# Performance work log

Measured on AMD Instinct MI355X. Metric: run time of the kernel, lower is better.

The kernel has to match this reference:

```python
import jax, jax.numpy as jnp
import numpy as np
from jax import lax

S, D_IN, D_FC, H_LSTM, H_RNN, D_OUT = 16384, 6, 20, 48, 24, 2


def _lstm_layer(seq, Wih, Whh, bih, bhh):
    # seq: [S, d_in]; PyTorch gate order: i, f, g, o
    H = Whh.shape[1]
    xW = seq @ Wih.T + (bih + bhh)  # [S, 4H] precomputed input projections

    def step(carry, xw):
        h, c = carry
        g = xw + h @ Whh.T
        i = jax.nn.sigmoid(g[:H])
        f = jax.nn.sigmoid(g[H:2 * H])
        gg = jnp.tanh(g[2 * H:3 * H])
        o = jax.nn.sigmoid(g[3 * H:])
        c = f * c + i * gg
        h = o * jnp.tanh(c)
        return (h, c), h

    z = jnp.zeros((H,), seq.dtype)
    _, hs = lax.scan(step, (z, z), xW)
    return hs  # [S, H]


def _rnn_layer(seq, Wih, Whh, bih, bhh):
    H = Whh.shape[1]
    xW = seq @ Wih.T + (bih + bhh)

    def step(h, xw):
        h = jnp.tanh(xw + h @ Whh.T)
        return h, h

    _, hs = lax.scan(step, jnp.zeros((H,), seq.dtype), xW)
    return hs


def setup_inputs() -> dict:
    key = jax.random.key(0)
    ks = iter(jax.random.split(key, 32))

    def p(shape, fan_in):
        s = 1.0 / np.sqrt(fan_in)
        return jax.random.uniform(next(ks), shape, jnp.float32, -s, s)

    inp = {"x": jax.random.normal(next(ks), (S, D_IN), jnp.float32)}
    inp["fc1_W"] = p((D_FC, D_IN), D_IN)
    inp["fc1_b"] = p((D_FC,), D_IN)
    inp["fc2_W"] = p((D_FC, D_FC), D_FC)
    inp["fc2_b"] = p((D_FC,), D_FC)
    # LSTM layer 0: input 20 -> hidden 48
    inp["lstm0_Wih"] = p((4 * H_LSTM, D_FC), H_LSTM)
    inp["lstm0_Whh"] = p((4 * H_LSTM, H_LSTM), H_LSTM)
    inp["lstm0_bih"] = p((4 * H_LSTM,), H_LSTM)
    inp["lstm0_bhh"] = p((4 * H_LSTM,), H_LSTM)
    # LSTM layers 1..4: input 48 -> hidden 48, stacked
    inp["lstmr_Wih"] = p((4, 4 * H_LSTM, H_LSTM), H_LSTM)
    inp["lstmr_Whh"] = p((4, 4 * H_LSTM, H_LSTM), H_LSTM)
    inp["lstmr_bih"] = p((4, 4 * H_LSTM), H_LSTM)
    inp["lstmr_bhh"] = p((4, 4 * H_LSTM), H_LSTM)
    # RNN layer 0: 48 -> 24, layer 1: 24 -> 24
    inp["rnn0_Wih"] = p((H_RNN, H_LSTM), H_RNN)
    inp["rnn0_Whh"] = p((H_RNN, H_RNN), H_RNN)
    inp["rnn0_bih"] = p((H_RNN,), H_RNN)
    inp["rnn0_bhh"] = p((H_RNN,), H_RNN)
    inp["rnn1_Wih"] = p((H_RNN, H_RNN), H_RNN)
    inp["rnn1_Whh"] = p((H_RNN, H_RNN), H_RNN)
    inp["rnn1_bih"] = p((H_RNN,), H_RNN)
    inp["rnn1_bhh"] = p((H_RNN,), H_RNN)
    inp["fc4_W"] = p((D_OUT, H_RNN), H_RNN)
    inp["fc4_b"] = p((D_OUT,), H_RNN)
    return inp


def reference(x, fc1_W, fc1_b, fc2_W, fc2_b,
              lstm0_Wih, lstm0_Whh, lstm0_bih, lstm0_bhh,
              lstmr_Wih, lstmr_Whh, lstmr_bih, lstmr_bhh,
              rnn0_Wih, rnn0_Whh, rnn0_bih, rnn0_bhh,
              rnn1_Wih, rnn1_Whh, rnn1_bih, rnn1_bhh,
              fc4_W, fc4_b):
    h = jax.nn.relu(x @ fc1_W.T + fc1_b)
    h = jax.nn.relu(h @ fc2_W.T + fc2_b)
    h = _lstm_layer(h, lstm0_Wih, lstm0_Whh, lstm0_bih, lstm0_bhh)
    for l in range(4):  # fixed small layer loop
        h = _lstm_layer(h, lstmr_Wih[l], lstmr_Whh[l], lstmr_bih[l], lstmr_bhh[l])
    h = _rnn_layer(h, rnn0_Wih, rnn0_Whh, rnn0_bih, rnn0_bhh)
    h = _rnn_layer(h, rnn1_Wih, rnn1_Whh, rnn1_bih, rnn1_bhh)
    h = jax.nn.relu(h)
    out = h @ fc4_W.T + fc4_b  # [S, 2]
    return out[None]  # [1, S, 2] matching batch_first torch output
```

## Files before the change

### kernel.cpp

```cpp
#include <hip/hip_runtime.h>
#include <hip/hip_bf16.h>

#define S_LEN 16384
#define N_IN 23
#define CH2 32
#define NCH2 (S_LEN / CH2)
#define RING_D 8

typedef float v2f __attribute__((ext_vector_type(2)));
typedef _Float16 h2v __attribute__((ext_vector_type(2)));

__device__ __forceinline__ float fsig(float x) {
    return __builtin_amdgcn_rcpf(1.f + __expf(-x));
}
__device__ __forceinline__ float ftanh_fast(float x) {
    float e = __expf(-2.f * fabsf(x));
    float r = (1.f - e) * __builtin_amdgcn_rcpf(1.f + e);
    return x >= 0.f ? r : -r;
}
__device__ __forceinline__ float rlane(float v, int k) {
    return __uint_as_float(__builtin_amdgcn_readlane(__float_as_uint(v), k));
}
__device__ __forceinline__ h2v rlane_h2(h2v v, int k) {
    int b;
    __builtin_memcpy(&b, &v, 4);
    b = __builtin_amdgcn_readlane(b, k);
    h2v r;
    __builtin_memcpy(&r, &b, 4);
    return r;
}
__device__ __forceinline__ h2v pack_h2(float a, float b) {
    auto p = __builtin_amdgcn_cvt_pkrtz(a, b);
    h2v r;
    __builtin_memcpy(&r, &p, 4);
    return r;
}
__device__ __forceinline__ float dpp_xor1(float v) {
    int b = __float_as_int(v);
    int r = __builtin_amdgcn_update_dpp(b, b, 0xB1, 0xF, 0xF, false);
    return __int_as_float(r);
}

#if __has_builtin(__builtin_amdgcn_fdot2)
__device__ __forceinline__ float fdot2_hw(h2v w, h2v h, float acc) {
    return __builtin_amdgcn_fdot2(w, h, acc, false);
}
#define FDOT2(w, h, acc) fdot2_hw((w), (h), (acc))
#else
__device__ __forceinline__ float fdot2_sw(h2v w, h2v h, float acc) {
    return acc + (float)w.x * (float)h.x + (float)w.y * (float)h.y;
}
#define FDOT2(w, h, acc) fdot2_sw((w), (h), (acc))
#endif

__global__ void detect_kernel(const void* probe, int nsamp, int* flag)
{
    if (blockIdx.x == 0 && threadIdx.x == 0) {
        const unsigned short* p = (const unsigned short*)probe;
        int isbf16 = 1;
        for (int i = 0; i < nsamp; i++) {
            float v = __uint_as_float(((unsigned int)p[i]) << 16);
            if (!(fabsf(v) < 1e4f)) { isbf16 = 0; break; }
        }
        *flag = isbf16;
    }
}

struct IngestArgs {
    const void* src[N_IN];
    float*      dst[N_IN];
    int         n[N_IN];
};

__global__ void ingest_kernel(IngestArgs args, const int* __restrict__ flag)
{
    const int isbf16 = *flag;
    const int tid    = blockIdx.x * blockDim.x + threadIdx.x;
    const int stride = gridDim.x * blockDim.x;
    for (int i = 0; i < N_IN; i++) {
        const int n = args.n[i];
        float* dst  = args.dst[i];
        if (isbf16) {
            const unsigned short* s = (const unsigned short*)args.src[i];
            for (int j = tid; j < n; j += stride)
                dst[j] = __uint_as_float(((unsigned int)s[j]) << 16);
        } else {
            const float* s = (const float*)args.src[i];
            for (int j = tid; j < n; j += stride)
                dst[j] = s[j];
        }
    }
}

__global__ void init_kernel(int* prog)
{
    int t = threadIdx.x;
    if (t < 1024) prog[t] = 0;
}

__global__ void fc12_kernel(const float* __restrict__ x,
                            const float* __restrict__ W1, const float* __restrict__ b1,
                            const float* __restrict__ W2, const float* __restrict__ b2,
                            float* __restrict__ h2out)
{
    int s = blockIdx.x * blockDim.x + threadIdx.x;
    if (s >= S_LEN) return;
    float xin[6];
#pragma unroll
    for (int k = 0; k < 6; k++) xin[k] = x[s * 6 + k];
    float h1[20];
#pragma unroll
    for (int j = 0; j < 20; j++) {
        float a = b1[j];
#pragma unroll
        for (int k = 0; k < 6; k++) a += W1[j * 6 + k] * xin[k];
        h1[j] = a > 0.f ? a : 0.f;
    }
#pragma unroll
    for (int j = 0; j < 20; j++) {
        float a = b2[j];
#pragma unroll
        for (int k = 0; k < 20; k++) a += W2[j * 20 + k] * h1[k];
        h2out[s * 20 + j] = a > 0.f ? a : 0.f;
    }
}

template <int DIN, int NG, bool TRANS>
__device__ void producer_block(const float* __restrict__ in,
                               const float* __restrict__ Wih,
                               const float* __restrict__ bih,
                               const float* __restrict__ bhh,
                               float* __restrict__ ring,
                               int* my_prog, int* in_prog, int* cons_prog,
                               float* smem)
{
    constexpr int GR  = NG / 3;
    constexpr int GS  = 256 / GR;
    constexpr int SLT = CH2 / GS;

    const int t  = threadIdx.x;
    const int rg = t % GR;
    const int sg = t / GR;

    float* in_sh = smem;
    float* xw_sh = smem + CH2 * DIN;

    float w[3][DIN];
    float bs[3];
    int cellr[3], partr[3];
#pragma unroll
    for (int r = 0; r < 3; r++) {
        const int row = rg * 3 + r;
#pragma unroll
        for (int k = 0; k < DIN; k++) w[r][k] = Wih[row * DIN + k];
        bs[r] = bih[row] + bhh[row];
        cellr[r] = row % 48;
        partr[r] = row / 48;
    }

    const float4* x4 = (const float4*)in_sh;

    for (int c = 0; c < NCH2; c++) {
        if (t == 0) {
            if (in_prog) {
                while (__hip_atomic_load(in_prog, __ATOMIC_ACQUIRE, __HIP_MEMORY_SCOPE_AGENT) < c + 1)
                    __builtin_amdgcn_s_sleep(1);
            }
            if (c >= RING_D) {
                while (__hip_atomic_load(cons_prog, __ATOMIC_ACQUIRE, __HIP_MEMORY_SCOPE_AGENT) < c - RING_D + 1)
                    __builtin_amdgcn_s_sleep(1);
            }
        }
        __syncthreads();
        {
            const float4* gsrc = (const float4*)(in + (size_t)c * CH2 * DIN);
            float4* ldst = (float4*)in_sh;
            for (int i = t; i < CH2 * DIN / 4; i += 256) ldst[i] = gsrc[i];
        }
        __syncthreads();

#pragma unroll
        for (int i = 0; i < SLT; i++) {
            const int sl = sg * SLT + i;
            float a0 = bs[0], a1 = bs[1], a2 = bs[2];
#pragma unroll
            for (int k = 0; k < DIN / 4; k++) {
                float4 xv = x4[sl * (DIN / 4) + k];
                a0 += w[0][4 * k + 0] * xv.x; a0 += w[0][4 * k + 1] * xv.y;
                a0 += w[0][4 * k + 2] * xv.z; a0 += w[0][4 * k + 3] * xv.w;
                a1 += w[1][4 * k + 0] * xv.x; a1 += w[1][4 * k + 1] * xv.y;
                a1 += w[1][4 * k + 2] * xv.z; a1 += w[1][4 * k + 3] * xv.w;
                a2 += w[2][4 * k + 0] * xv.x; a2 += w[2][4 * k + 1] * xv.y;
                a2 += w[2][4 * k + 2] * xv.z; a2 += w[2][4 * k + 3] * xv.w;
            }
            if (TRANS) {
                xw_sh[(sl * 48 + cellr[0]) * 4 + partr[0]] = a0;
                xw_sh[(sl * 48 + cellr[1]) * 4 + partr[1]] = a1;
                xw_sh[(sl * 48 + cellr[2]) * 4 + partr[2]] = a2;
            } else {
                xw_sh[sl * NG + rg * 3 + 0] = a0;
                xw_sh[sl * NG + rg * 3 + 1] = a1;
                xw_sh[sl * NG + rg * 3 + 2] = a2;
            }
        }
        __syncthreads();
        {
            const float4* lsrc = (const float4*)xw_sh;
            float4* gdst = (float4*)(ring + (size_t)(c % RING_D) * CH2 * NG);
            for (int i = t; i < CH2 * NG / 4; i += 256) gdst[i] = lsrc[i];
        }
        __syncthreads();
        if (t == 0)
            __hip_atomic_store(my_prog, c + 1, __ATOMIC_RELEASE, __HIP_MEMORY_SCOPE_AGENT);
    }
}

__device__ void lstm_scan(const float* __restrict__ Whh,
                          const float* __restrict__ ring,
                          float* __restrict__ hseq,
                          int* my_prog, int* prod_prog, float* smem)
{
    const int t = threadIdx.x;
    const int j = (t < 48) ? t : 47;
    float* xw_buf = smem;
    float* hh_buf = smem + 12288;

    h2v wI[24], wF[24], wG[24], wO[24];
    if (t < 64) {
#pragma unroll
        for (int k = 0; k < 24; k++) {
            wI[k] = pack_h2(Whh[j * 48 + 2 * k],         Whh[j * 48 + 2 * k + 1]);
            wF[k] = pack_h2(Whh[(48 + j) * 48 + 2 * k],  Whh[(48 + j) * 48 + 2 * k + 1]);
            wG[k] = pack_h2(Whh[(96 + j) * 48 + 2 * k],  Whh[(96 + j) * 48 + 2 * k + 1]);
            wO[k] = pack_h2(Whh[(144 + j) * 48 + 2 * k], Whh[(144 + j) * 48 + 2 * k + 1]);
        }
    }
    float hvec = 0.f, ccell = 0.f;

    if (t >= 128) {
        while (__hip_atomic_load(prod_prog, __ATOMIC_ACQUIRE, __HIP_MEMORY_SCOPE_AGENT) < 1)
            __builtin_amdgcn_s_sleep(8);
        const float4* g = (const float4*)ring;
        float4* d = (float4*)xw_buf;
        for (int i = t - 128; i < CH2 * 48; i += 128) d[i] = g[i];
    }
    __syncthreads();

    for (int c = 0; c < NCH2; c++) {
        if (t < 64) {
            const float4* xf = (const float4*)(xw_buf + (c & 1) * (CH2 * 192));
            float* hh = hh_buf + (c & 1) * (CH2 * 48);
            float4 xw4 = xf[j];
            for (int sl = 0; sl < CH2; sl++) {
                float4 nxt = xf[(sl + 1 < CH2 ? sl + 1 : sl) * 48 + j];
                float hn = dpp_xor1(hvec);
                h2v hp = pack_h2(hvec, hn);
                float aI0 = xw4.x, aF0 = xw4.y, aG0 = xw4.z, aO0 = xw4.w;
                float aI1 = 0.f, aF1 = 0.f, aG1 = 0.f, aO1 = 0.f;
#pragma unroll
                for (int kp = 0; kp < 12; kp++) {
                    h2v hb = rlane_h2(hp, 2 * kp);
                    aI0 = FDOT2(wI[kp], hb, aI0);
                    aF0 = FDOT2(wF[kp], hb, aF0);
                    aG0 = FDOT2(wG[kp], hb, aG0);
                    aO0 = FDOT2(wO[kp], hb, aO0);
                }
#pragma unroll
                for (int kp = 12; kp < 24; kp++) {
                    h2v hb = rlane_h2(hp, 2 * kp);
                    aI1 = FDOT2(wI[kp], hb, aI1);
                    aF1 = FDOT2(wF[kp], hb, aF1);
                    aG1 = FDOT2(wG[kp], hb, aG1);
                    aO1 = FDOT2(wO[kp], hb, aO1);
                }
                float iv = fsig(aI0 + aI1);
                float fv = fsig(aF0 + aF1);
                float gv = 2.f * fsig(2.f * (aG0 + aG1)) - 1.f;
                ccell = fv * ccell + iv * gv;
                float eO = __expf(-(aO0 + aO1));
                float eC = __expf(-2.f * fabsf(ccell));
                float r  = (1.f - eC) * __builtin_amdgcn_rcpf((1.f + eO) * (1.f + eC));
                float h  = __int_as_float(__float_as_int(r) ^
                                          (__float_as_int(ccell) & 0x80000000));
                hvec = h;
                if (t < 48) hh[sl * 48 + t] = h;
                xw4 = nxt;
            }
        } else if (t < 128) {
            if (c >= 1) {
                const float4* s4 = (const float4*)(hh_buf + ((c - 1) & 1) * (CH2 * 48));
                float4* d4 = (float4*)(hseq + (size_t)(c - 1) * CH2 * 48);
                for (int i = t - 64; i < CH2 * 12; i += 64) d4[i] = s4[i];
                if (t == 64)
                    __hip_atomic_store(my_prog, c, __ATOMIC_RELEASE, __HIP_MEMORY_SCOPE_AGENT);
            }
        } else {
            if (c + 1 < NCH2) {
                while (__hip_atomic_load(prod_prog, __ATOMIC_ACQUIRE, __HIP_MEMORY_SCOPE_AGENT) < c + 2)
                    __builtin_amdgcn_s_sleep(8);
                const float4* g = (const float4*)(ring + (size_t)((c + 1) % RING_D) * CH2 * 192);
                float4* d = (float4*)(xw_buf + ((c + 1) & 1) * (CH2 * 192));
                for (int i = t - 128; i < CH2 * 48; i += 128) d[i] = g[i];
            }
        }
        __syncthreads();
    }
    if (t >= 64 && t < 128) {
        const float4* s4 = (const float4*)(hh_buf + ((NCH2 - 1) & 1) * (CH2 * 48));
        float4* d4 = (float4*)(hseq + (size_t)(NCH2 - 1) * CH2 * 48);
        for (int i = t - 64; i < CH2 * 12; i += 64) d4[i] = s4[i];
        if (t == 64)
            __hip_atomic_store(my_prog, NCH2, __ATOMIC_RELEASE, __HIP_MEMORY_SCOPE_AGENT);
    }
}

__device__ void rnn_scan(const float* __restrict__ Whh,
                         const float* __restrict__ ring,
                         float* __restrict__ hseq,
                         int* my_prog, int* prod_prog, float* smem)
{
    const int t = threadIdx.x;
    float* xw_buf = smem;
    float* hh_buf = smem + 1536;

    float whh[24];
    if (t < 24) {
#pragma unroll
        for (int k = 0; k < 24; k++) whh[k] = Whh[t * 24 + k];
    }
    float hvec = 0.f;

    if (t >= 128) {
        while (__hip_atomic_load(prod_prog, __ATOMIC_ACQUIRE, __HIP_MEMORY_SCOPE_AGENT) < 1)
            __builtin_amdgcn_s_sleep(8);
        const float4* g = (const float4*)ring;
        float4* d = (float4*)xw_buf;
        for (int i = t - 128; i < CH2 * 6; i += 128) d[i] = g[i];
    }
    __syncthreads();

    for (int c = 0; c < NCH2; c++) {
        if (t < 64) {
            const float* xwc = xw_buf + (c & 1) * (CH2 * 24);
            float* hh = hh_buf + (c & 1) * (CH2 * 24);
            float xwv = (t < 24) ? xwc[t] : 0.f;
            for (int sl = 0; sl < CH2; sl++) {
                float nxtx = (t < 24) ? xwc[((sl + 1 < CH2) ? sl + 1 : sl) * 24 + t] : 0.f;
                float a0 = xwv, a1 = 0.f, a2 = 0.f, a3 = 0.f;
#pragma unroll
                for (int k = 0; k < 24; k += 4) {
                    a0 += rlane(hvec, k + 0) * whh[k + 0];
                    a1 += rlane(hvec, k + 1) * whh[k + 1];
                    a2 += rlane(hvec, k + 2) * whh[k + 2];
                    a3 += rlane(hvec, k + 3) * whh[k + 3];
                }
                float h = ftanh_fast((a0 + a1) + (a2 + a3));
                if (t < 24) {
                    hvec = h;
                    hh[sl * 24 + t] = h;
                }
                xwv = nxtx;
            }
        } else if (t < 128) {
            if (c >= 1) {
                const float4* s4 = (const float4*)(hh_buf + ((c - 1) & 1) * (CH2 * 24));
                float4* d4 = (float4*)(hseq + (size_t)(c - 1) * CH2 * 24);
                for (int i = t - 64; i < CH2 * 6; i += 64) d4[i] = s4[i];
                if (t == 64)
                    __hip_atomic_store(my_prog, c, __ATOMIC_RELEASE, __HIP_MEMORY_SCOPE_AGENT);
            }
        } else {
            if (c + 1 < NCH2) {
                while (__hip_atomic_load(prod_prog, __ATOMIC_ACQUIRE, __HIP_MEMORY_SCOPE_AGENT) < c + 2)
                    __builtin_amdgcn_s_sleep(8);
                const float4* g = (const float4*)(ring + (size_t)((c + 1) % RING_D) * CH2 * 24);
                float4* d = (float4*)(xw_buf + ((c + 1) & 1) * (CH2 * 24));
                for (int i = t - 128; i < CH2 * 6; i += 128) d[i] = g[i];
            }
        }
        __syncthreads();
    }
    if (t >= 64 && t < 128) {
        const float4* s4 = (const float4*)(hh_buf + ((NCH2 - 1) & 1) * (CH2 * 24));
        float4* d4 = (float4*)(hseq + (size_t)(NCH2 - 1) * CH2 * 24);
        for (int i = t - 64; i < CH2 * 6; i += 64) d4[i] = s4[i];
        if (t == 64)
            __hip_atomic_store(my_prog, NCH2, __ATOMIC_RELEASE, __HIP_MEMORY_SCOPE_AGENT);
    }
}

struct PipeArgs {
    const float* h2;
    const float* l0_Wih; const float* l0_Whh; const float* l0_bih; const float* l0_bhh;
    const float* lr_Wih; const float* lr_Whh; const float* lr_bih; const float* lr_bhh;
    const float* r0_Wih; const float* r0_Whh; const float* r0_bih; const float* r0_bhh;
    const float* r1_Wih; const float* r1_Whh; const float* r1_bih; const float* r1_bhh;
    float* seq0; float* seq1; float* seq2; float* seq3; float* seq4;
    float* rnnA; float* rnnB;
    float* ring[7];
    int* prog;
};

__global__ void __launch_bounds__(256, 1) pipeline_kernel(PipeArgs a)
{
    __shared__ __align__(16) float smem[15360];
    const int b = blockIdx.x;
    const float* seqin[7] = {a.h2, a.seq0, a.seq1, a.seq2, a.seq3, a.seq4, a.rnnA};
    float* seqout[7] = {a.seq0, a.seq1, a.seq2, a.seq3, a.seq4, a.rnnA, a.rnnB};
    int* sp[7]; int* pp[7];
    for (int l = 0; l < 7; l++) { sp[l] = a.prog + l * 64; pp[l] = a.prog + (8 + l) * 64; }

    if (b < 7) {
        const int l = b;
        int* inp = (l == 0) ? nullptr : sp[l - 1];
        if (l == 0) {
            producer_block<20, 192, true>(a.h2, a.l0_Wih, a.l0_bih, a.l0_bhh,
                                          a.ring[0], pp[0], inp, sp[0], smem);
        } else if (l <= 4) {
            producer_block<48, 192, true>(seqin[l],
                                          a.lr_Wih + (size_t)(l - 1) * 192 * 48,
                                          a.lr_bih + (size_t)(l - 1) * 192,
                                          a.lr_bhh + (size_t)(l - 1) * 192,
                                          a.ring[l], pp[l], inp, sp[l], smem);
        } else if (l == 5) {
            producer_block<48, 24, false>(a.seq4, a.r0_Wih, a.r0_bih, a.r0_bhh,
                                          a.ring[5], pp[5], inp, sp[5], smem);
        } else {
            producer_block<24, 24, false>(a.rnnA, a.r1_Wih, a.r1_bih, a.r1_bhh,
                                          a.ring[6], pp[6], inp, sp[6], smem);
        }
    } else {
        const int l = b - 7;
        if (l == 0) {
            lstm_scan(a.l0_Whh, a.ring[0], seqout[0], sp[0], pp[0], smem);
        } else if (l <= 4) {
            lstm_scan(a.lr_Whh + (size_t)(l - 1) * 192 * 48,
                      a.ring[l], seqout[l], sp[l], pp[l], smem);
        } else if (l == 5) {
            rnn_scan(a.r0_Whh, a.ring[5], seqout[5], sp[5], pp[5], smem);
        } else {
            rnn_scan(a.r1_Whh, a.ring[6], seqout[6], sp[6], pp[6], smem);
        }
    }
}

__global__ void out_kernel(const float* __restrict__ hin,
                           const float* __restrict__ W,
                           const float* __restrict__ b,
                           void* __restrict__ out,
                           const int* __restrict__ flag)
{
    int s = blockIdx.x * blockDim.x + threadIdx.x;
    if (s >= S_LEN) return;
    const int isbf16 = *flag;
    float h[24];
#pragma unroll
    for (int k = 0; k < 24; k++) {
        float v = hin[s * 24 + k];
        h[k] = v > 0.f ? v : 0.f;
    }
#pragma unroll
    for (int j = 0; j < 2; j++) {
        float a = b[j];
#pragma unroll
        for (int k = 0; k < 24; k++) a += W[j * 24 + k] * h[k];
        if (isbf16) ((__hip_bfloat16*)out)[s * 2 + j] = __float2bfloat16(a);
        else        ((float*)out)[s * 2 + j] = a;
    }
}

extern "C" void kernel_launch(void* const* d_in, const int* in_sizes, int n_in,
                              void* d_out, int out_size, void* d_ws, size_t ws_size,
                              hipStream_t stream)
{
    int*   ip    = (int*)d_ws;
    int*   flag  = ip;
    int*   prog  = ip + 256;
    float* ws    = (float*)d_ws;
    float* conv0 = ws + 4096;

    IngestArgs ia;
    float* conv[N_IN];
    {
        float* p = conv0;
        for (int i = 0; i < N_IN; i++) {
            conv[i] = p;
            ia.src[i] = d_in[i];
            ia.dst[i] = p;
            ia.n[i]   = in_sizes[i];
            p += in_sizes[i];
        }
    }
    float* h2   = conv0 + 191000;
    float* seq0 = h2 + 327680;
    float* seq1 = seq0 + 786432;
    float* seq2 = seq1 + 786432;
    float* seq3 = seq2 + 786432;
    float* seq4 = seq3 + 786432;
    float* rnnA = seq4 + 786432;
    float* rnnB = rnnA + 393216;
    float* rbase = rnnB + 393216;
    float* ring[7];
    {
        float* p = rbase;
        for (int l = 0; l < 5; l++) { ring[l] = p; p += RING_D * CH2 * 192; }
        for (int l = 5; l < 7; l++) { ring[l] = p; p += RING_D * CH2 * 24;  }
    }

    const int TPB = 256;
    const int NB  = S_LEN / TPB;

    detect_kernel<<<1, 64, 0, stream>>>(d_in[1], in_sizes[1], flag);
    ingest_kernel<<<128, 256, 0, stream>>>(ia, flag);
    init_kernel<<<1, 1024, 0, stream>>>(prog);

    fc12_kernel<<<NB, TPB, 0, stream>>>(conv[0], conv[1], conv[2], conv[3], conv[4], h2);

    PipeArgs pa;
    pa.h2 = h2;
    pa.l0_Wih = conv[5];  pa.l0_Whh = conv[6];  pa.l0_bih = conv[7];  pa.l0_bhh = conv[8];
    pa.lr_Wih = conv[9];  pa.lr_Whh = conv[10]; pa.lr_bih = conv[11]; pa.lr_bhh = conv[12];
    pa.r0_Wih = conv[13]; pa.r0_Whh = conv[14]; pa.r0_bih = conv[15]; pa.r0_bhh = conv[16];
    pa.r1_Wih = conv[17]; pa.r1_Whh = conv[18]; pa.r1_bih = conv[19]; pa.r1_bhh = conv[20];
    pa.seq0 = seq0; pa.seq1 = seq1; pa.seq2 = seq2; pa.seq3 = seq3; pa.seq4 = seq4;
    pa.rnnA = rnnA; pa.rnnB = rnnB;
    for (int l = 0; l < 7; l++) pa.ring[l] = ring[l];
    pa.prog = prog;

    pipeline_kernel<<<14, 256, 0, stream>>>(pa);

    out_kernel<<<NB, TPB, 0, stream>>>(rnnB, conv[21], conv[22], d_out, flag);
}
```

Measured before the change: 5.604 ms.

## Fold log2e scaling into LSTM weights, use exp2, and pad xw LDS layout

Pre-multiplies the input and recurrent LSTM weights and biases by log2(e) (twice that for the g gate) so the serial recurrence can call hardware exp2 directly. It also merges the i and g gate reciprocals into one rcp. Separately, it pads the shared-memory xw buffer by one float4 every 16 entries to avoid LDS bank conflicts, which grows shared memory. The goal is fewer instructions on the latency-bound recurrent critical path, at the cost of extra fp16 rounding on the scaled weights.

```diff
diff --git a/kernel.cpp b/kernel.cpp
--- a/kernel.cpp
+++ b/kernel.cpp
@@ -7,9 +7,21 @@
 #define NCH2 (S_LEN / CH2)
 #define RING_D 8
 
+#define XW_PAR_F4 1632
+#define XW_FLOATS (2 * XW_PAR_F4 * 4)
+#define L2E   1.442695041f
+#define TWO_L2E 2.885390082f
+
 typedef float v2f __attribute__((ext_vector_type(2)));
 typedef _Float16 h2v __attribute__((ext_vector_type(2)));
 
+__device__ __forceinline__ float fexp2(float x) {
+#if __has_builtin(__builtin_amdgcn_exp2f)
+    return __builtin_amdgcn_exp2f(x);
+#else
+    return exp2f(x);
+#endif
+}
 __device__ __forceinline__ float fsig(float x) {
     return __builtin_amdgcn_rcpf(1.f + __expf(-x));
 }
@@ -151,9 +163,10 @@
 #pragma unroll
     for (int r = 0; r < 3; r++) {
         const int row = rg * 3 + r;
-#pragma unroll
-        for (int k = 0; k < DIN; k++) w[r][k] = Wih[row * DIN + k];
-        bs[r] = bih[row] + bhh[row];
+        const float fac = TRANS ? ((row / 48) == 2 ? TWO_L2E : L2E) : 1.f;
+#pragma unroll
+        for (int k = 0; k < DIN; k++) w[r][k] = Wih[row * DIN + k] * fac;
+        bs[r] = (bih[row] + bhh[row]) * fac;
         cellr[r] = row % 48;
         partr[r] = row / 48;
     }
@@ -223,18 +236,19 @@
     const int t = threadIdx.x;
     const int j = (t < 48) ? t : 47;
     float* xw_buf = smem;
-    float* hh_buf = smem + 12288;
+    float* hh_buf = smem + XW_FLOATS;
 
     h2v wI[24], wF[24], wG[24], wO[24];
     if (t < 64) {
 #pragma unroll
         for (int k = 0; k < 24; k++) {
-            wI[k] = pack_h2(Whh[j * 48 + 2 * k],         Whh[j * 48 + 2 * k + 1]);
-            wF[k] = pack_h2(Whh[(48 + j) * 48 + 2 * k],  Whh[(48 + j) * 48 + 2 * k + 1]);
-            wG[k] = pack_h2(Whh[(96 + j) * 48 + 2 * k],  Whh[(96 + j) * 48 + 2 * k + 1]);
-            wO[k] = pack_h2(Whh[(144 + j) * 48 + 2 * k], Whh[(144 + j) * 48 + 2 * k + 1]);
-        }
-    }
+            wI[k] = pack_h2(Whh[j * 48 + 2 * k] * L2E,           Whh[j * 48 + 2 * k + 1] * L2E);
+            wF[k] = pack_h2(Whh[(48 + j) * 48 + 2 * k] * L2E,    Whh[(48 + j) * 48 + 2 * k + 1] * L2E);
+            wG[k] = pack_h2(Whh[(96 + j) * 48 + 2 * k] * TWO_L2E, Whh[(96 + j) * 48 + 2 * k + 1] * TWO_L2E);
+            wO[k] = pack_h2(Whh[(144 + j) * 48 + 2 * k] * L2E,   Whh[(144 + j) * 48 + 2 * k + 1] * L2E);
+        }
+    }
+    const int jo = j + (j >> 4);
     float hvec = 0.f, ccell = 0.f;
 
     if (t >= 128) {
@@ -242,17 +256,17 @@
             __builtin_amdgcn_s_sleep(8);
         const float4* g = (const float4*)ring;
         float4* d = (float4*)xw_buf;
-        for (int i = t - 128; i < CH2 * 48; i += 128) d[i] = g[i];
+        for (int i = t - 128; i < CH2 * 48; i += 128) d[i + (i >> 4)] = g[i];
     }
     __syncthreads();
 
     for (int c = 0; c < NCH2; c++) {
         if (t < 64) {
-            const float4* xf = (const float4*)(xw_buf + (c & 1) * (CH2 * 192));
+            const float4* xf = (const float4*)xw_buf + (c & 1) * XW_PAR_F4;
             float* hh = hh_buf + (c & 1) * (CH2 * 48);
-            float4 xw4 = xf[j];
+            float4 xw4 = xf[jo];
             for (int sl = 0; sl < CH2; sl++) {
-                float4 nxt = xf[(sl + 1 < CH2 ? sl + 1 : sl) * 48 + j];
+                float4 nxt = xf[(sl + 1) * 51 + jo];
                 float hn = dpp_xor1(hvec);
                 h2v hp = pack_h2(hvec, hn);
                 float aI0 = xw4.x, aF0 = xw4.y, aG0 = xw4.z, aO0 = xw4.w;
@@ -273,12 +287,18 @@
                     aG1 = FDOT2(wG[kp], hb, aG1);
                     aO1 = FDOT2(wO[kp], hb, aO1);
                 }
-                float iv = fsig(aI0 + aI1);
-                float fv = fsig(aF0 + aF1);
-                float gv = 2.f * fsig(2.f * (aG0 + aG1)) - 1.f;
-                ccell = fv * ccell + iv * gv;
-                float eO = __expf(-(aO0 + aO1));
-                float eC = __expf(-2.f * fabsf(ccell));
+                float aI = aI0 + aI1, aF = aF0 + aF1;
+                float aG = aG0 + aG1, aO = aO0 + aO1;
+                float eI = fexp2(-aI);
+                float eF = fexp2(-aF);
+                float eG = fexp2(-fabsf(aG));
+                float eO = fexp2(-aO);
+                float fv = __builtin_amdgcn_rcpf(1.f + eF);
+                float ig = (1.f - eG) * __builtin_amdgcn_rcpf((1.f + eI) * (1.f + eG));
+                ig = __int_as_float(__float_as_int(ig) ^
+                                    (__float_as_int(aG) & 0x80000000));
+                ccell = fmaf(fv, ccell, ig);
+                float eC = fexp2(-TWO_L2E * fabsf(ccell));
                 float r  = (1.f - eC) * __builtin_amdgcn_rcpf((1.f + eO) * (1.f + eC));
                 float h  = __int_as_float(__float_as_int(r) ^
                                           (__float_as_int(ccell) & 0x80000000));
@@ -299,8 +319,8 @@
                 while (__hip_atomic_load(prod_prog, __ATOMIC_ACQUIRE, __HIP_MEMORY_SCOPE_AGENT) < c + 2)
                     __builtin_amdgcn_s_sleep(8);
                 const float4* g = (const float4*)(ring + (size_t)((c + 1) % RING_D) * CH2 * 192);
-                float4* d = (float4*)(xw_buf + ((c + 1) & 1) * (CH2 * 192));
-                for (int i = t - 128; i < CH2 * 48; i += 128) d[i] = g[i];
+                float4* d = (float4*)xw_buf + ((c + 1) & 1) * XW_PAR_F4;
+                for (int i = t - 128; i < CH2 * 48; i += 128) d[i + (i >> 4)] = g[i];
             }
         }
         __syncthreads();
@@ -403,7 +423,7 @@
 
 __global__ void __launch_bounds__(256, 1) pipeline_kernel(PipeArgs a)
 {
-    __shared__ __align__(16) float smem[15360];
+    __shared__ __align__(16) float smem[16128];
     const int b = blockIdx.x;
     const float* seqin[7] = {a.h2, a.seq0, a.seq1, a.seq2, a.seq3, a.seq4, a.rnnA};
     float* seqout[7] = {a.seq0, a.seq1, a.seq2, a.seq3, a.seq4, a.rnnA, a.rnnB};
```

Measured after the change: 5.536 ms. Within noise of the previous version (-1.2%).
